# Kernel tuning notes

Measured on AMD Instinct MI355X. Metric: run time of the kernel, lower is better.

The kernel has to match this reference:

```python
import jax, jax.numpy as jnp
import numpy as np

N = 50000       # num_nodes
E = 800000      # num_edges (avg degree 16)
IN, HID, OUT = 128, 128, 128
ALPHA = 0.5
EPS = 1e-5      # torch BatchNorm1d default eps


def _lin_init(k, fan_in, fan_out):
    # mimic torch nn.Linear default init: U(-1/sqrt(fan_in), 1/sqrt(fan_in))
    s = 1.0 / np.sqrt(fan_in)
    kw, kb = jax.random.split(k)
    W = jax.random.uniform(kw, (fan_out, fan_in), jnp.float32, -s, s)
    b = jax.random.uniform(kb, (fan_out,), jnp.float32, -s, s)
    return W, b


def setup_inputs() -> dict:
    key = jax.random.key(0)
    ks = jax.random.split(key, 6)
    x = jax.random.normal(ks[0], (N, IN), jnp.float32)
    edge_index = jax.random.randint(ks[1], (2, E), 0, N, dtype=jnp.int64)
    W1, b1 = _lin_init(ks[2], IN, HID)
    W2, b2 = _lin_init(ks[3], HID, HID)
    W3, b3 = _lin_init(ks[4], HID, OUT)
    g1 = jnp.ones((HID,), jnp.float32); bt1 = jnp.zeros((HID,), jnp.float32)
    g2 = jnp.ones((HID,), jnp.float32); bt2 = jnp.zeros((HID,), jnp.float32)
    return {"x": x, "edge_index": edge_index,
            "W1": W1, "b1": b1, "W2": W2, "b2": b2, "W3": W3, "b3": b3,
            "g1": g1, "bt1": bt1, "g2": g2, "bt2": bt2}


def _high_pass(h, row, col):
    # (I - alpha * A_norm) h, with GCN-style symmetric normalization
    # deg computed from row (source) indices, as in the torch code.
    deg = jax.ops.segment_sum(jnp.ones((E,), h.dtype), row, num_segments=N)
    dinv = jnp.where(deg > 0, deg ** -0.5, 0.0)   # [N]
    norm = dinv[row] * dinv[col]                  # [E]
    agg = jax.ops.segment_sum(h[col] * norm[:, None], row, num_segments=N)
    return h - ALPHA * agg


def _bn(h, g, b):
    # BatchNorm1d in training mode: batch statistics (biased variance)
    m = h.mean(axis=0)
    v = h.var(axis=0)
    return (h - m) * jax.lax.rsqrt(v + EPS) * g + b


def reference(x, edge_index, W1, b1, W2, b2, W3, b3, g1, bt1, g2, bt2):
    row, col = edge_index[0], edge_index[1]
    # layer 0
    h = _high_pass(x, row, col)
    h = h @ W1.T + b1
    h = jax.nn.relu(_bn(h, g1, bt1))  # dropout is identity at eval
    # layer 1
    h = _high_pass(h, row, col)
    h = h @ W2.T + b2
    h = jax.nn.relu(_bn(h, g2, bt2))
    # layer 2 (output)
    h = _high_pass(h, row, col)
    h = h @ W3.T + b3
    return h
```

## Files before the change

### kernel.cpp

```cpp
#include <hip/hip_runtime.h>
#include <hip/hip_fp16.h>

#define N_NODES 50000
#define N_EDGES 800000
#define F 128
#define ALPHA 0.5f
#define BN_EPS 1e-5f
#define NB_SCAN ((N_NODES + 255) / 256)
#define GEMM_NBLK ((N_NODES + 63) / 64)
#define NGRP 8
#define GRP_ROWS (N_NODES / NGRP)
#define NCHUNK 64
#define CHUNK_I4 (N_EDGES / NCHUNK / 4)
#define PREP_THREADS 1024
#define NB_X2H ((N_NODES * F / 8 + PREP_THREADS - 1) / PREP_THREADS)
#define NB_PB 6
#define NB_HIST (NGRP * NCHUNK)

typedef _Float16 half8_t __attribute__((ext_vector_type(8)));
typedef float floatx4 __attribute__((ext_vector_type(4)));

union H8 { uint4 u; __half2 h2[4]; };

__global__ __launch_bounds__(PREP_THREADS) void prep_kernel(
        const float* __restrict__ x, __half* __restrict__ xh,
        const float* __restrict__ W1, const float* __restrict__ W2,
        const float* __restrict__ W3, _Float16* __restrict__ Bp,
        const int* __restrict__ row, int* __restrict__ subhist) {
    int bid = blockIdx.x;
    if (bid < NB_X2H) {
        int idx = bid * PREP_THREADS + threadIdx.x;
        if (idx < N_NODES * F / 8) {
            float4 f0 = ((const float4*)x)[idx * 2];
            float4 f1 = ((const float4*)x)[idx * 2 + 1];
            H8 o;
            o.h2[0] = __float22half2_rn(make_float2(f0.x, f0.y));
            o.h2[1] = __float22half2_rn(make_float2(f0.z, f0.w));
            o.h2[2] = __float22half2_rn(make_float2(f1.x, f1.y));
            o.h2[3] = __float22half2_rn(make_float2(f1.z, f1.w));
            ((uint4*)xh)[idx] = o.u;
        }
    } else if (bid < NB_X2H + NB_PB) {
        int idx = (bid - NB_X2H) * PREP_THREADS + threadIdx.x;
        int layer = idx >> 11;
        int r = idx & 2047;
        int t = r >> 6, lane = r & 63;
        int s = t >> 3, n0 = t & 7;
        int n = n0 * 16 + (lane & 15);
        int k = s * 32 + (lane >> 4) * 8;
        const float* W = (layer == 0) ? W1 : (layer == 1) ? W2 : W3;
        float4 f0 = *(const float4*)(W + n * 128 + k);
        float4 f1 = *(const float4*)(W + n * 128 + k + 4);
        _Float16* dst = Bp + (size_t)layer * 32768 + (size_t)r * 8;
        dst[0] = (_Float16)f0.x; dst[1] = (_Float16)f0.y;
        dst[2] = (_Float16)f0.z; dst[3] = (_Float16)f0.w;
        dst[4] = (_Float16)f1.x; dst[5] = (_Float16)f1.y;
        dst[6] = (_Float16)f1.z; dst[7] = (_Float16)f1.w;
    } else {
        int t = bid - (NB_X2H + NB_PB);
        int g = t & 7, c = t >> 3;
        int rlo = g * GRP_ROWS;
        __shared__ int hist[GRP_ROWS];
        for (int j = threadIdx.x; j < GRP_ROWS; j += PREP_THREADS) hist[j] = 0;
        __syncthreads();
        const int4* r4 = (const int4*)row;
        for (int v = c * CHUNK_I4 + threadIdx.x; v < (c + 1) * CHUNK_I4;
             v += PREP_THREADS) {
            int4 rr = r4[v];
            if ((unsigned)(rr.x - rlo) < GRP_ROWS) atomicAdd(&hist[rr.x - rlo], 1);
            if ((unsigned)(rr.y - rlo) < GRP_ROWS) atomicAdd(&hist[rr.y - rlo], 1);
            if ((unsigned)(rr.z - rlo) < GRP_ROWS) atomicAdd(&hist[rr.z - rlo], 1);
            if ((unsigned)(rr.w - rlo) < GRP_ROWS) atomicAdd(&hist[rr.w - rlo], 1);
        }
        __syncthreads();
        for (int j = threadIdx.x; j < GRP_ROWS; j += PREP_THREADS)
            subhist[(size_t)c * N_NODES + rlo + j] = hist[j];
    }
}


__global__ void scan_block(int* __restrict__ subhist, int* __restrict__ localscan,
                           int* __restrict__ blocksum, float* __restrict__ dinv) {
    __shared__ int s[256];
    int i = blockIdx.x * 256 + threadIdx.x;
    int deg = 0;
    if (i < N_NODES) {
        for (int c = 0; c < NCHUNK; ++c) {
            int t = subhist[(size_t)c * N_NODES + i];
            subhist[(size_t)c * N_NODES + i] = deg;
            deg += t;
        }
        dinv[i] = deg > 0 ? rsqrtf((float)deg) : 0.f;
    }
    s[threadIdx.x] = deg;
    __syncthreads();
    for (int off = 1; off < 256; off <<= 1) {
        int t = (threadIdx.x >= off) ? s[threadIdx.x - off] : 0;
        __syncthreads();
        s[threadIdx.x] += t;
        __syncthreads();
    }
    if (i < N_NODES) localscan[i] = s[threadIdx.x];
    if (threadIdx.x == 255) blocksum[blockIdx.x] = s[255];
}

__global__ void scan_add_tops(const int* __restrict__ localscan,
                              const int* __restrict__ blocksum,
                              int* __restrict__ rowptr) {
    __shared__ int s[256];
    int v = (threadIdx.x < NB_SCAN) ? blocksum[threadIdx.x] : 0;
    s[threadIdx.x] = v;
    __syncthreads();
    for (int off = 1; off < 256; off <<= 1) {
        int t = (threadIdx.x >= off) ? s[threadIdx.x - off] : 0;
        __syncthreads();
        s[threadIdx.x] += t;
        __syncthreads();
    }
    int base = (blockIdx.x > 0) ? s[blockIdx.x - 1] : 0;
    int i = blockIdx.x * 256 + threadIdx.x;
    if (i < N_NODES) rowptr[i + 1] = localscan[i] + base;
    if (i == 0) rowptr[0] = 0;
}


__global__ __launch_bounds__(PREP_THREADS) void fill_kernel(
        const int* __restrict__ row, const int* __restrict__ col,
        const int* __restrict__ rowptr, const int* __restrict__ chunkoff,
        const float* __restrict__ dinv, unsigned int* __restrict__ colwt) {
    int t = blockIdx.x;
    int g = t & 7, c = t >> 3;
    int rlo = g * GRP_ROWS;
    __shared__ int cur[GRP_ROWS];
    for (int j = threadIdx.x; j < GRP_ROWS; j += PREP_THREADS)
        cur[j] = rowptr[rlo + j] + chunkoff[(size_t)c * N_NODES + rlo + j];
    __syncthreads();
    const int4* r4 = (const int4*)row;
    const int4* c4 = (const int4*)col;
    for (int v = c * CHUNK_I4 + threadIdx.x; v < (c + 1) * CHUNK_I4;
         v += PREP_THREADS) {
        int4 rr = r4[v];
        int4 cc = c4[v];
        int rs[4] = {rr.x, rr.y, rr.z, rr.w};
        int cs[4] = {cc.x, cc.y, cc.z, cc.w};
        #pragma unroll
        for (int k = 0; k < 4; ++k) {
            if ((unsigned)(rs[k] - rlo) < GRP_ROWS) {
                int pos = atomicAdd(&cur[rs[k] - rlo], 1);
                unsigned int hb = __half_as_ushort(__float2half(dinv[cs[k]]));
                colwt[pos] = (unsigned int)cs[k] | (hb << 16);
            }
        }
    }
}

template <int USEBN>
__global__ __launch_bounds__(256) void hp_kernel(
        const __half* __restrict__ h,
        const float* __restrict__ scale, const float* __restrict__ shift,
        const float* __restrict__ dinv, const int* __restrict__ rowptr,
        const unsigned int* __restrict__ colwt, __half* __restrict__ out) {
    int lane = threadIdx.x & 63;
    int q = lane >> 4;
    int l = lane & 15;
    int i = blockIdx.x * 4 + (threadIdx.x >> 6);

    float sc[8], sh[8];
    if (USEBN) {
        float4 a0 = ((const float4*)scale)[l * 2];
        float4 a1 = ((const float4*)scale)[l * 2 + 1];
        float4 b0 = ((const float4*)shift)[l * 2];
        float4 b1 = ((const float4*)shift)[l * 2 + 1];
        sc[0] = a0.x; sc[1] = a0.y; sc[2] = a0.z; sc[3] = a0.w;
        sc[4] = a1.x; sc[5] = a1.y; sc[6] = a1.z; sc[7] = a1.w;
        sh[0] = b0.x; sh[1] = b0.y; sh[2] = b0.z; sh[3] = b0.w;
        sh[4] = b1.x; sh[5] = b1.y; sh[6] = b1.z; sh[7] = b1.w;
    }

    int e0 = rowptr[i], e1 = rowptr[i + 1];
    const char* hb = (const char*)h;
    int loff = l * 16;
    float acc[8] = {0.f, 0.f, 0.f, 0.f, 0.f, 0.f, 0.f, 0.f};

    int e = e0 + q;
    for (; e + 4 < e1; e += 8) {
        unsigned int cw0 = colwt[e];
        unsigned int cw1 = colwt[e + 4];
        H8 r0, r1;
        r0.u = *(const uint4*)(hb + (size_t)(cw0 & 0xffffu) * 256 + loff);
        r1.u = *(const uint4*)(hb + (size_t)(cw1 & 0xffffu) * 256 + loff);
        float w0 = __half2float(__ushort_as_half((unsigned short)(cw0 >> 16)));
        float w1 = __half2float(__ushort_as_half((unsigned short)(cw1 >> 16)));
        #pragma unroll
        for (int p = 0; p < 4; ++p) {
            float2 f0 = __half22float2(r0.h2[p]);
            float2 f1 = __half22float2(r1.h2[p]);
            if (USEBN) {
                f0.x = fmaxf(fmaf(f0.x, sc[2 * p], sh[2 * p]), 0.f);
                f0.y = fmaxf(fmaf(f0.y, sc[2 * p + 1], sh[2 * p + 1]), 0.f);
                f1.x = fmaxf(fmaf(f1.x, sc[2 * p], sh[2 * p]), 0.f);
                f1.y = fmaxf(fmaf(f1.y, sc[2 * p + 1], sh[2 * p + 1]), 0.f);
            }
            acc[2 * p]     = fmaf(w0, f0.x, acc[2 * p]);
            acc[2 * p + 1] = fmaf(w0, f0.y, acc[2 * p + 1]);
            acc[2 * p]     = fmaf(w1, f1.x, acc[2 * p]);
            acc[2 * p + 1] = fmaf(w1, f1.y, acc[2 * p + 1]);
        }
    }
    for (; e < e1; e += 4) {
        unsigned int cw = colwt[e];
        H8 r0;
        r0.u = *(const uint4*)(hb + (size_t)(cw & 0xffffu) * 256 + loff);
        float w0 = __half2float(__ushort_as_half((unsigned short)(cw >> 16)));
        #pragma unroll
        for (int p = 0; p < 4; ++p) {
            float2 f0 = __half22float2(r0.h2[p]);
            if (USEBN) {
                f0.x = fmaxf(fmaf(f0.x, sc[2 * p], sh[2 * p]), 0.f);
                f0.y = fmaxf(fmaf(f0.y, sc[2 * p + 1], sh[2 * p + 1]), 0.f);
            }
            acc[2 * p]     = fmaf(w0, f0.x, acc[2 * p]);
            acc[2 * p + 1] = fmaf(w0, f0.y, acc[2 * p + 1]);
        }
    }

    #pragma unroll
    for (int c = 0; c < 8; ++c) {
        acc[c] += __shfl_xor(acc[c], 16);
        acc[c] += __shfl_xor(acc[c], 32);
    }

    float a = ALPHA * dinv[i];
    if (q == 0) {
        H8 s8, o;
        s8.u = *(const uint4*)(hb + (size_t)i * 256 + loff);
        #pragma unroll
        for (int p = 0; p < 4; ++p) {
            float2 f = __half22float2(s8.h2[p]);
            if (USEBN) {
                f.x = fmaxf(fmaf(f.x, sc[2 * p], sh[2 * p]), 0.f);
                f.y = fmaxf(fmaf(f.y, sc[2 * p + 1], sh[2 * p + 1]), 0.f);
            }
            o.h2[p] = __float22half2_rn(
                make_float2(f.x - a * acc[2 * p], f.y - a * acc[2 * p + 1]));
        }
        *(uint4*)((char*)out + (size_t)i * 256 + loff) = o.u;
    }
}

template <int MODE>
__global__ __launch_bounds__(256) void gemm_kernel(
        const __half* __restrict__ A, const _Float16* __restrict__ Bp,
        const float* __restrict__ bias, void* __restrict__ outv,
        float* __restrict__ partial, int M) {
    __shared__ float st_s[4][128];
    __shared__ float st_q[4][128];
    int tid = threadIdx.x;
    int w = tid >> 6, lane = tid & 63;
    int l = lane & 15, g = lane >> 4;
    int row0 = blockIdx.x * 64 + w * 16;
    bool active = row0 < M;

    const char* Ab = (const char*)A;
    half8_t a[4];
    if (active) {
        #pragma unroll
        for (int s = 0; s < 4; ++s)
            a[s] = *(const half8_t*)(Ab + (size_t)(row0 + l) * 256 + s * 64 + g * 16);
    } else {
        half8_t z = 0;
        a[0] = z; a[1] = z; a[2] = z; a[3] = z;
    }

    #pragma unroll
    for (int n0 = 0; n0 < 8; ++n0) {
        floatx4 acc = {0.f, 0.f, 0.f, 0.f};
        #pragma unroll
        for (int s = 0; s < 4; ++s) {
            half8_t b = *(const half8_t*)(Bp + ((size_t)(s * 8 + n0) * 64 + lane) * 8);
            acc = __builtin_amdgcn_mfma_f32_16x16x32_f16(a[s], b, acc, 0, 0, 0);
        }
        int col = n0 * 16 + l;
        float bv = bias[col];
        float v0 = acc[0] + bv, v1 = acc[1] + bv, v2 = acc[2] + bv, v3 = acc[3] + bv;
        if (active) {
            int r = row0 + g * 4;
            if (MODE == 0) {
                __half* oh = (__half*)outv;
                oh[(size_t)r * 128 + col]       = __float2half_rn(v0);
                oh[(size_t)(r + 1) * 128 + col] = __float2half_rn(v1);
                oh[(size_t)(r + 2) * 128 + col] = __float2half_rn(v2);
                oh[(size_t)(r + 3) * 128 + col] = __float2half_rn(v3);
            } else {
                float* of = (float*)outv;
                of[(size_t)r * 128 + col]       = v0;
                of[(size_t)(r + 1) * 128 + col] = v1;
                of[(size_t)(r + 2) * 128 + col] = v2;
                of[(size_t)(r + 3) * 128 + col] = v3;
            }
        } else {
            v0 = v1 = v2 = v3 = 0.f;
        }
        if (MODE == 0) {
            float s_ = v0 + v1 + v2 + v3;
            float q_ = v0 * v0 + v1 * v1 + v2 * v2 + v3 * v3;
            s_ += __shfl_xor(s_, 16); s_ += __shfl_xor(s_, 32);
            q_ += __shfl_xor(q_, 16); q_ += __shfl_xor(q_, 32);
            if (lane < 16) { st_s[w][col] = s_; st_q[w][col] = q_; }
        }
    }
    if (MODE == 0) {
        __syncthreads();
        if (tid < 128) {
            partial[(size_t)blockIdx.x * 256 + tid] =
                st_s[0][tid] + st_s[1][tid] + st_s[2][tid] + st_s[3][tid];
            partial[(size_t)blockIdx.x * 256 + 128 + tid] =
                st_q[0][tid] + st_q[1][tid] + st_q[2][tid] + st_q[3][tid];
        }
    }
}

__global__ __launch_bounds__(256) void bn_reduce_kernel(
        const float* __restrict__ partial,
        const float* __restrict__ g, const float* __restrict__ bt,
        float* __restrict__ scale, float* __restrict__ shift) {
    __shared__ float ss[256], sq[256];
    int j = blockIdx.x;
    int tid = threadIdx.x;
    float s = 0.f, q = 0.f;
    for (int b = tid; b < GEMM_NBLK; b += 256) {
        s += partial[(size_t)b * 256 + j];
        q += partial[(size_t)b * 256 + 128 + j];
    }
    ss[tid] = s; sq[tid] = q;
    __syncthreads();
    for (int off = 128; off > 0; off >>= 1) {
        if (tid < off) { ss[tid] += ss[tid + off]; sq[tid] += sq[tid + off]; }
        __syncthreads();
    }
    if (tid == 0) {
        float m = ss[0] / (float)N_NODES;
        float v = sq[0] / (float)N_NODES - m * m;
        float sc = g[j] * rsqrtf(v + BN_EPS);
        scale[j] = sc;
        shift[j] = bt[j] - m * sc;
    }
}


extern "C" void kernel_launch(void* const* d_in, const int* in_sizes, int n_in,
                              void* d_out, int out_size, void* d_ws, size_t ws_size,
                              hipStream_t stream) {
    const float* x   = (const float*)d_in[0];
    const int*   ei  = (const int*)d_in[1];
    const float* W1  = (const float*)d_in[2];
    const float* b1  = (const float*)d_in[3];
    const float* W2  = (const float*)d_in[4];
    const float* b2  = (const float*)d_in[5];
    const float* W3  = (const float*)d_in[6];
    const float* b3  = (const float*)d_in[7];
    const float* g1  = (const float*)d_in[8];
    const float* bt1 = (const float*)d_in[9];
    const float* g2  = (const float*)d_in[10];
    const float* bt2 = (const float*)d_in[11];
    float* out = (float*)d_out;

    const int* row = ei;
    const int* col = ei + N_EDGES;

    char* ws = (char*)d_ws;
    size_t off = 0;
    auto alloc = [&](size_t bytes) -> void* {
        void* p = ws + off;
        off += (bytes + 255) & ~(size_t)255;
        return p;
    };
    int*   rowptr   = (int*)alloc((N_NODES + 1) * 4);
    int*   localscan= (int*)alloc(N_NODES * 4);
    int*   blocksum = (int*)alloc(NB_SCAN * 4);
    float* dinv     = (float*)alloc(N_NODES * 4);
    unsigned int* colwt = (unsigned int*)alloc((size_t)N_EDGES * 4);
    _Float16* Bp    = (_Float16*)alloc(3 * 32768 * 2);
    float* partial  = (float*)alloc((size_t)GEMM_NBLK * 256 * 4);
    float* scale1   = (float*)alloc(F * 4);
    float* shift1   = (float*)alloc(F * 4);
    float* scale2   = (float*)alloc(F * 4);
    float* shift2   = (float*)alloc(F * 4);
    __half* xh      = (__half*)alloc((size_t)N_NODES * F * 2);
    __half* hpA     = (__half*)alloc((size_t)(N_NODES + 64) * F * 2);
    __half* hB      = (__half*)alloc((size_t)N_NODES * F * 2);
    int* subhist    = (int*)hB;
    (void)ws_size; (void)n_in; (void)in_sizes; (void)out_size;

    prep_kernel<<<NB_X2H + NB_PB + NB_HIST, PREP_THREADS, 0, stream>>>(
        x, xh, W1, W2, W3, Bp, row, subhist);
    scan_block<<<NB_SCAN, 256, 0, stream>>>(subhist, localscan, blocksum, dinv);
    scan_add_tops<<<NB_SCAN, 256, 0, stream>>>(localscan, blocksum, rowptr);
    fill_kernel<<<NB_HIST, PREP_THREADS, 0, stream>>>(row, col, rowptr, subhist,
                                                      dinv, colwt);

    const int hp_grid = N_NODES / 4;

    hp_kernel<0><<<hp_grid, 256, 0, stream>>>(xh, nullptr, nullptr, dinv, rowptr,
                                              colwt, hpA);
    gemm_kernel<0><<<GEMM_NBLK, 256, 0, stream>>>(hpA, Bp, b1, hB, partial, N_NODES);
    bn_reduce_kernel<<<128, 256, 0, stream>>>(partial, g1, bt1, scale1, shift1);

    hp_kernel<1><<<hp_grid, 256, 0, stream>>>(hB, scale1, shift1, dinv, rowptr,
                                              colwt, hpA);
    gemm_kernel<0><<<GEMM_NBLK, 256, 0, stream>>>(hpA, Bp + 32768, b2, hB, partial,
                                                  N_NODES);
    bn_reduce_kernel<<<128, 256, 0, stream>>>(partial, g2, bt2, scale2, shift2);

    hp_kernel<1><<<hp_grid, 256, 0, stream>>>(hB, scale2, shift2, dinv, rowptr,
                                              colwt, hpA);
    gemm_kernel<1><<<GEMM_NBLK, 256, 0, stream>>>(hpA, Bp + 65536, b3, out, nullptr,
                                                  N_NODES);
}
```

Before: 190.8 us.

## Fuse high-pass aggregation with MFMA GEMM through an LDS tile

Merges each layer's sparse high-pass gather and the following dense GEMM into one kernel. Each block aggregates 64 rows, with each wave handling 16 rows in turn, and writes them into a swizzled shared-memory tile that feeds the MFMA GEMM directly. This removes the fp16 intermediate buffer round trip through global memory and one launch per layer. The gather loop is also unrolled to four edges per lane. The cost is far fewer waves in flight (one block per 64 rows instead of per 4 rows), which may reduce latency hiding for the irregular gathers.

```diff
diff --git a/kernel.cpp b/kernel.cpp
--- a/kernel.cpp
+++ b/kernel.cpp
@@ -154,137 +154,164 @@
     }
 }
 
-template <int USEBN>
-__global__ __launch_bounds__(256) void hp_kernel(
+template <int USEBN, int MODE>
+__global__ __launch_bounds__(256) void fused_kernel(
         const __half* __restrict__ h,
         const float* __restrict__ scale, const float* __restrict__ shift,
         const float* __restrict__ dinv, const int* __restrict__ rowptr,
-        const unsigned int* __restrict__ colwt, __half* __restrict__ out) {
-    int lane = threadIdx.x & 63;
-    int q = lane >> 4;
-    int l = lane & 15;
-    int i = blockIdx.x * 4 + (threadIdx.x >> 6);
-
-    float sc[8], sh[8];
-    if (USEBN) {
-        float4 a0 = ((const float4*)scale)[l * 2];
-        float4 a1 = ((const float4*)scale)[l * 2 + 1];
-        float4 b0 = ((const float4*)shift)[l * 2];
-        float4 b1 = ((const float4*)shift)[l * 2 + 1];
-        sc[0] = a0.x; sc[1] = a0.y; sc[2] = a0.z; sc[3] = a0.w;
-        sc[4] = a1.x; sc[5] = a1.y; sc[6] = a1.z; sc[7] = a1.w;
-        sh[0] = b0.x; sh[1] = b0.y; sh[2] = b0.z; sh[3] = b0.w;
-        sh[4] = b1.x; sh[5] = b1.y; sh[6] = b1.z; sh[7] = b1.w;
-    }
-
-    int e0 = rowptr[i], e1 = rowptr[i + 1];
-    const char* hb = (const char*)h;
-    int loff = l * 16;
-    float acc[8] = {0.f, 0.f, 0.f, 0.f, 0.f, 0.f, 0.f, 0.f};
-
-    int e = e0 + q;
-    for (; e + 4 < e1; e += 8) {
-        unsigned int cw0 = colwt[e];
-        unsigned int cw1 = colwt[e + 4];
-        H8 r0, r1;
-        r0.u = *(const uint4*)(hb + (size_t)(cw0 & 0xffffu) * 256 + loff);
-        r1.u = *(const uint4*)(hb + (size_t)(cw1 & 0xffffu) * 256 + loff);
-        float w0 = __half2float(__ushort_as_half((unsigned short)(cw0 >> 16)));
-        float w1 = __half2float(__ushort_as_half((unsigned short)(cw1 >> 16)));
-        #pragma unroll
-        for (int p = 0; p < 4; ++p) {
-            float2 f0 = __half22float2(r0.h2[p]);
-            float2 f1 = __half22float2(r1.h2[p]);
-            if (USEBN) {
-                f0.x = fmaxf(fmaf(f0.x, sc[2 * p], sh[2 * p]), 0.f);
-                f0.y = fmaxf(fmaf(f0.y, sc[2 * p + 1], sh[2 * p + 1]), 0.f);
-                f1.x = fmaxf(fmaf(f1.x, sc[2 * p], sh[2 * p]), 0.f);
-                f1.y = fmaxf(fmaf(f1.y, sc[2 * p + 1], sh[2 * p + 1]), 0.f);
-            }
-            acc[2 * p]     = fmaf(w0, f0.x, acc[2 * p]);
-            acc[2 * p + 1] = fmaf(w0, f0.y, acc[2 * p + 1]);
-            acc[2 * p]     = fmaf(w1, f1.x, acc[2 * p]);
-            acc[2 * p + 1] = fmaf(w1, f1.y, acc[2 * p + 1]);
-        }
-    }
-    for (; e < e1; e += 4) {
-        unsigned int cw = colwt[e];
-        H8 r0;
-        r0.u = *(const uint4*)(hb + (size_t)(cw & 0xffffu) * 256 + loff);
-        float w0 = __half2float(__ushort_as_half((unsigned short)(cw >> 16)));
-        #pragma unroll
-        for (int p = 0; p < 4; ++p) {
-            float2 f0 = __half22float2(r0.h2[p]);
-            if (USEBN) {
-                f0.x = fmaxf(fmaf(f0.x, sc[2 * p], sh[2 * p]), 0.f);
-                f0.y = fmaxf(fmaf(f0.y, sc[2 * p + 1], sh[2 * p + 1]), 0.f);
-            }
-            acc[2 * p]     = fmaf(w0, f0.x, acc[2 * p]);
-            acc[2 * p + 1] = fmaf(w0, f0.y, acc[2 * p + 1]);
-        }
-    }
-
-    #pragma unroll
-    for (int c = 0; c < 8; ++c) {
-        acc[c] += __shfl_xor(acc[c], 16);
-        acc[c] += __shfl_xor(acc[c], 32);
-    }
-
-    float a = ALPHA * dinv[i];
-    if (q == 0) {
-        H8 s8, o;
-        s8.u = *(const uint4*)(hb + (size_t)i * 256 + loff);
-        #pragma unroll
-        for (int p = 0; p < 4; ++p) {
-            float2 f = __half22float2(s8.h2[p]);
-            if (USEBN) {
-                f.x = fmaxf(fmaf(f.x, sc[2 * p], sh[2 * p]), 0.f);
-                f.y = fmaxf(fmaf(f.y, sc[2 * p + 1], sh[2 * p + 1]), 0.f);
-            }
-            o.h2[p] = __float22half2_rn(
-                make_float2(f.x - a * acc[2 * p], f.y - a * acc[2 * p + 1]));
-        }
-        *(uint4*)((char*)out + (size_t)i * 256 + loff) = o.u;
-    }
-}
-
-template <int MODE>
-__global__ __launch_bounds__(256) void gemm_kernel(
-        const __half* __restrict__ A, const _Float16* __restrict__ Bp,
-        const float* __restrict__ bias, void* __restrict__ outv,
-        float* __restrict__ partial, int M) {
+        const unsigned int* __restrict__ colwt,
+        const _Float16* __restrict__ Bp, const float* __restrict__ bias,
+        void* __restrict__ outv, float* __restrict__ partial) {
+    __shared__ uint4 sA[64 * 16];
     __shared__ float st_s[4][128];
     __shared__ float st_q[4][128];
     int tid = threadIdx.x;
     int w = tid >> 6, lane = tid & 63;
-    int l = lane & 15, g = lane >> 4;
+    int q = lane >> 4, l = lane & 15;
     int row0 = blockIdx.x * 64 + w * 16;
-    bool active = row0 < M;
-
-    const char* Ab = (const char*)A;
-    half8_t a[4];
+    bool active = row0 < N_NODES;
+
+    const char* hb = (const char*)h;
+    int loff = l * 16;
+
     if (active) {
-        #pragma unroll
-        for (int s = 0; s < 4; ++s)
-            a[s] = *(const half8_t*)(Ab + (size_t)(row0 + l) * 256 + s * 64 + g * 16);
-    } else {
-        half8_t z = 0;
-        a[0] = z; a[1] = z; a[2] = z; a[3] = z;
-    }
-
-    #pragma unroll
-    for (int n0 = 0; n0 < 8; ++n0) {
-        floatx4 acc = {0.f, 0.f, 0.f, 0.f};
+        float sc[8], sh[8];
+        if (USEBN) {
+            float4 a0 = ((const float4*)scale)[l * 2];
+            float4 a1 = ((const float4*)scale)[l * 2 + 1];
+            float4 b0 = ((const float4*)shift)[l * 2];
+            float4 b1 = ((const float4*)shift)[l * 2 + 1];
+            sc[0] = a0.x; sc[1] = a0.y; sc[2] = a0.z; sc[3] = a0.w;
+            sc[4] = a1.x; sc[5] = a1.y; sc[6] = a1.z; sc[7] = a1.w;
+            sh[0] = b0.x; sh[1] = b0.y; sh[2] = b0.z; sh[3] = b0.w;
+            sh[4] = b1.x; sh[5] = b1.y; sh[6] = b1.z; sh[7] = b1.w;
+        }
+        for (int rr = 0; rr < 16; ++rr) {
+            int i = row0 + rr;
+            int e0 = rowptr[i], e1 = rowptr[i + 1];
+            float acc[8] = {0.f, 0.f, 0.f, 0.f, 0.f, 0.f, 0.f, 0.f};
+            int e = e0 + q;
+            for (; e + 14 < e1; e += 16) {
+                unsigned int cw0 = colwt[e];
+                unsigned int cw1 = colwt[e + 4];
+                unsigned int cw2 = colwt[e + 8];
+                unsigned int cw3 = colwt[e + 12];
+                H8 r0, r1, r2, r3;
+                r0.u = *(const uint4*)(hb + (size_t)(cw0 & 0xffffu) * 256 + loff);
+                r1.u = *(const uint4*)(hb + (size_t)(cw1 & 0xffffu) * 256 + loff);
+                r2.u = *(const uint4*)(hb + (size_t)(cw2 & 0xffffu) * 256 + loff);
+                r3.u = *(const uint4*)(hb + (size_t)(cw3 & 0xffffu) * 256 + loff);
+                float w0 = __half2float(__ushort_as_half((unsigned short)(cw0 >> 16)));
+                float w1 = __half2float(__ushort_as_half((unsigned short)(cw1 >> 16)));
+                float w2 = __half2float(__ushort_as_half((unsigned short)(cw2 >> 16)));
+                float w3 = __half2float(__ushort_as_half((unsigned short)(cw3 >> 16)));
+                #pragma unroll
+                for (int p = 0; p < 4; ++p) {
+                    float2 f0 = __half22float2(r0.h2[p]);
+                    float2 f1 = __half22float2(r1.h2[p]);
+                    float2 f2 = __half22float2(r2.h2[p]);
+                    float2 f3 = __half22float2(r3.h2[p]);
+                    if (USEBN) {
+                        f0.x = fmaxf(fmaf(f0.x, sc[2 * p], sh[2 * p]), 0.f);
+                        f0.y = fmaxf(fmaf(f0.y, sc[2 * p + 1], sh[2 * p + 1]), 0.f);
+                        f1.x = fmaxf(fmaf(f1.x, sc[2 * p], sh[2 * p]), 0.f);
+                        f1.y = fmaxf(fmaf(f1.y, sc[2 * p + 1], sh[2 * p + 1]), 0.f);
+                        f2.x = fmaxf(fmaf(f2.x, sc[2 * p], sh[2 * p]), 0.f);
+                        f2.y = fmaxf(fmaf(f2.y, sc[2 * p + 1], sh[2 * p + 1]), 0.f);
+                        f3.x = fmaxf(fmaf(f3.x, sc[2 * p], sh[2 * p]), 0.f);
+                        f3.y = fmaxf(fmaf(f3.y, sc[2 * p + 1], sh[2 * p + 1]), 0.f);
+                    }
+                    acc[2 * p]     = fmaf(w0, f0.x, acc[2 * p]);
+                    acc[2 * p + 1] = fmaf(w0, f0.y, acc[2 * p + 1]);
+                    acc[2 * p]     = fmaf(w1, f1.x, acc[2 * p]);
+                    acc[2 * p + 1] = fmaf(w1, f1.y, acc[2 * p + 1]);
+                    acc[2 * p]     = fmaf(w2, f2.x, acc[2 * p]);
+                    acc[2 * p + 1] = fmaf(w2, f2.y, acc[2 * p + 1]);
+                    acc[2 * p]     = fmaf(w3, f3.x, acc[2 * p]);
+                    acc[2 * p + 1] = fmaf(w3, f3.y, acc[2 * p + 1]);
+                }
+            }
+            for (; e + 6 < e1; e += 8) {
+                unsigned int cw0 = colwt[e];
+                unsigned int cw1 = colwt[e + 4];
+                H8 r0, r1;
+                r0.u = *(const uint4*)(hb + (size_t)(cw0 & 0xffffu) * 256 + loff);
+                r1.u = *(const uint4*)(hb + (size_t)(cw1 & 0xffffu) * 256 + loff);
+                float w0 = __half2float(__ushort_as_half((unsigned short)(cw0 >> 16)));
+                float w1 = __half2float(__ushort_as_half((unsigned short)(cw1 >> 16)));
+                #pragma unroll
+                for (int p = 0; p < 4; ++p) {
+                    float2 f0 = __half22float2(r0.h2[p]);
+                    float2 f1 = __half22float2(r1.h2[p]);
+                    if (USEBN) {
+                        f0.x = fmaxf(fmaf(f0.x, sc[2 * p], sh[2 * p]), 0.f);
+                        f0.y = fmaxf(fmaf(f0.y, sc[2 * p + 1], sh[2 * p + 1]), 0.f);
+                        f1.x = fmaxf(fmaf(f1.x, sc[2 * p], sh[2 * p]), 0.f);
+                        f1.y = fmaxf(fmaf(f1.y, sc[2 * p + 1], sh[2 * p + 1]), 0.f);
+                    }
+                    acc[2 * p]     = fmaf(w0, f0.x, acc[2 * p]);
+                    acc[2 * p + 1] = fmaf(w0, f0.y, acc[2 * p + 1]);
+                    acc[2 * p]     = fmaf(w1, f1.x, acc[2 * p]);
+                    acc[2 * p + 1] = fmaf(w1, f1.y, acc[2 * p + 1]);
+                }
+            }
+            for (; e < e1; e += 4) {
+                unsigned int cw = colwt[e];
+                H8 r0;
+                r0.u = *(const uint4*)(hb + (size_t)(cw & 0xffffu) * 256 + loff);
+                float w0 = __half2float(__ushort_as_half((unsigned short)(cw >> 16)));
+                #pragma unroll
+                for (int p = 0; p < 4; ++p) {
+                    float2 f0 = __half22float2(r0.h2[p]);
+                    if (USEBN) {
+                        f0.x = fmaxf(fmaf(f0.x, sc[2 * p], sh[2 * p]), 0.f);
+                        f0.y = fmaxf(fmaf(f0.y, sc[2 * p + 1], sh[2 * p + 1]), 0.f);
+                    }
+                    acc[2 * p]     = fmaf(w0, f0.x, acc[2 * p]);
+                    acc[2 * p + 1] = fmaf(w0, f0.y, acc[2 * p + 1]);
+                }
+            }
+            #pragma unroll
+            for (int c = 0; c < 8; ++c) {
+                acc[c] += __shfl_xor(acc[c], 16);
+                acc[c] += __shfl_xor(acc[c], 32);
+            }
+            if (q == 0) {
+                float a = ALPHA * dinv[i];
+                H8 s8, o;
+                s8.u = *(const uint4*)(hb + (size_t)i * 256 + loff);
+                #pragma unroll
+                for (int p = 0; p < 4; ++p) {
+                    float2 f = __half22float2(s8.h2[p]);
+                    if (USEBN) {
+                        f.x = fmaxf(fmaf(f.x, sc[2 * p], sh[2 * p]), 0.f);
+                        f.y = fmaxf(fmaf(f.y, sc[2 * p + 1], sh[2 * p + 1]), 0.f);
+                    }
+                    o.h2[p] = __float22half2_rn(
+                        make_float2(f.x - a * acc[2 * p], f.y - a * acc[2 * p + 1]));
+                }
+                sA[(w * 16 + rr) * 16 + (l ^ (rr & 7))] = o.u;
+            }
+        }
+        int g2 = lane >> 4;
+        half8_t a[4];
         #pragma unroll
         for (int s = 0; s < 4; ++s) {
-            half8_t b = *(const half8_t*)(Bp + ((size_t)(s * 8 + n0) * 64 + lane) * 8);
-            acc = __builtin_amdgcn_mfma_f32_16x16x32_f16(a[s], b, acc, 0, 0, 0);
-        }
-        int col = n0 * 16 + l;
-        float bv = bias[col];
-        float v0 = acc[0] + bv, v1 = acc[1] + bv, v2 = acc[2] + bv, v3 = acc[3] + bv;
-        if (active) {
-            int r = row0 + g * 4;
+            int chunk = (s * 4 + g2) ^ (l & 7);
+            a[s] = *(const half8_t*)&sA[(w * 16 + l) * 16 + chunk];
+        }
+        #pragma unroll
+        for (int n0 = 0; n0 < 8; ++n0) {
+            floatx4 acc = {0.f, 0.f, 0.f, 0.f};
+            #pragma unroll
+            for (int s = 0; s < 4; ++s) {
+                half8_t b = *(const half8_t*)(Bp + ((size_t)(s * 8 + n0) * 64 + lane) * 8);
+                acc = __builtin_amdgcn_mfma_f32_16x16x32_f16(a[s], b, acc, 0, 0, 0);
+            }
+            int col = n0 * 16 + l;
+            float bv = bias[col];
+            float v0 = acc[0] + bv, v1 = acc[1] + bv, v2 = acc[2] + bv, v3 = acc[3] + bv;
+            int r = row0 + g2 * 4;
             if (MODE == 0) {
                 __half* oh = (__half*)outv;
                 oh[(size_t)r * 128 + col]       = __float2half_rn(v0);
@@ -298,15 +325,21 @@
                 of[(size_t)(r + 2) * 128 + col] = v2;
                 of[(size_t)(r + 3) * 128 + col] = v3;
             }
-        } else {
-            v0 = v1 = v2 = v3 = 0.f;
-        }
-        if (MODE == 0) {
-            float s_ = v0 + v1 + v2 + v3;
-            float q_ = v0 * v0 + v1 * v1 + v2 * v2 + v3 * v3;
-            s_ += __shfl_xor(s_, 16); s_ += __shfl_xor(s_, 32);
-            q_ += __shfl_xor(q_, 16); q_ += __shfl_xor(q_, 32);
-            if (lane < 16) { st_s[w][col] = s_; st_q[w][col] = q_; }
+            if (MODE == 0) {
+                float s_ = v0 + v1 + v2 + v3;
+                float q_ = v0 * v0 + v1 * v1 + v2 * v2 + v3 * v3;
+                s_ += __shfl_xor(s_, 16); s_ += __shfl_xor(s_, 32);
+                q_ += __shfl_xor(q_, 16); q_ += __shfl_xor(q_, 32);
+                if (lane < 16) { st_s[w][col] = s_; st_q[w][col] = q_; }
+            }
+        }
+    } else if (MODE == 0) {
+        if (lane < 16) {
+            #pragma unroll
+            for (int n0 = 0; n0 < 8; ++n0) {
+                st_s[w][n0 * 16 + l] = 0.f;
+                st_q[w][n0 * 16 + l] = 0.f;
+            }
         }
     }
     if (MODE == 0) {
@@ -387,9 +420,9 @@
     float* scale2   = (float*)alloc(F * 4);
     float* shift2   = (float*)alloc(F * 4);
     __half* xh      = (__half*)alloc((size_t)N_NODES * F * 2);
-    __half* hpA     = (__half*)alloc((size_t)(N_NODES + 64) * F * 2);
-    __half* hB      = (__half*)alloc((size_t)N_NODES * F * 2);
-    int* subhist    = (int*)hB;
+    __half* h1      = (__half*)alloc((size_t)N_NODES * F * 2);
+    __half* h2      = (__half*)alloc((size_t)N_NODES * F * 2);
+    int* subhist    = (int*)h1;
     (void)ws_size; (void)n_in; (void)in_sizes; (void)out_size;
 
     prep_kernel<<<NB_X2H + NB_PB + NB_HIST, PREP_THREADS, 0, stream>>>(
@@ -399,21 +432,14 @@
     fill_kernel<<<NB_HIST, PREP_THREADS, 0, stream>>>(row, col, rowptr, subhist,
                                                       dinv, colwt);
 
-    const int hp_grid = N_NODES / 4;
-
-    hp_kernel<0><<<hp_grid, 256, 0, stream>>>(xh, nullptr, nullptr, dinv, rowptr,
-                                              colwt, hpA);
-    gemm_kernel<0><<<GEMM_NBLK, 256, 0, stream>>>(hpA, Bp, b1, hB, partial, N_NODES);
+    fused_kernel<0, 0><<<GEMM_NBLK, 256, 0, stream>>>(
+        xh, nullptr, nullptr, dinv, rowptr, colwt, Bp, b1, h1, partial);
     bn_reduce_kernel<<<128, 256, 0, stream>>>(partial, g1, bt1, scale1, shift1);
 
-    hp_kernel<1><<<hp_grid, 256, 0, stream>>>(hB, scale1, shift1, dinv, rowptr,
-                                              colwt, hpA);
-    gemm_kernel<0><<<GEMM_NBLK, 256, 0, stream>>>(hpA, Bp + 32768, b2, hB, partial,
-                                                  N_NODES);
+    fused_kernel<1, 0><<<GEMM_NBLK, 256, 0, stream>>>(
+        h1, scale1, shift1, dinv, rowptr, colwt, Bp + 32768, b2, h2, partial);
     bn_reduce_kernel<<<128, 256, 0, stream>>>(partial, g2, bt2, scale2, shift2);
 
-    hp_kernel<1><<<hp_grid, 256, 0, stream>>>(hB, scale2, shift2, dinv, rowptr,
-                                              colwt, hpA);
-    gemm_kernel<1><<<GEMM_NBLK, 256, 0, stream>>>(hpA, Bp + 65536, b3, out, nullptr,
-                                                  N_NODES);
-}
+    fused_kernel<1, 1><<<GEMM_NBLK, 256, 0, stream>>>(
+        h2, scale2, shift2, dinv, rowptr, colwt, Bp + 65536, b3, out, nullptr);
+}
```

Result: slower. 239.0 us (+25.3%).

## Split node features into 32-column planes so neighbor gathers stay L2-resident

Applied to the files above, without the earlier changes.

Stores the half-precision feature matrices as four column planes of 32 features each. The prep, hp and gemm kernels all index the new layout. The hp grid now runs tile-major, so each aggregation pass gathers from a single 3.2 MB plane that can stay resident in L2, and each wave processes 16 edges at a time with 64-byte rows. The goal is to cut DRAM/L2 misses from the random neighbor gather. In exchange, the CSR index and weight arrays are read four times per layer, and gathers use smaller 64-byte row segments.

```diff
diff --git a/kernel.cpp b/kernel.cpp
--- a/kernel.cpp
+++ b/kernel.cpp
@@ -16,6 +16,10 @@
 #define NB_X2H ((N_NODES * F / 8 + PREP_THREADS - 1) / PREP_THREADS)
 #define NB_PB 6
 #define NB_HIST (NGRP * NCHUNK)
+#define NTILE 4
+#define TILE_C 32
+#define PLANE_H ((size_t)N_NODES * TILE_C)
+#define NRB (N_NODES / 4)
 
 typedef _Float16 half8_t __attribute__((ext_vector_type(8)));
 typedef float floatx4 __attribute__((ext_vector_type(4)));
@@ -31,6 +35,8 @@
     if (bid < NB_X2H) {
         int idx = bid * PREP_THREADS + threadIdx.x;
         if (idx < N_NODES * F / 8) {
+            int i = idx >> 4;
+            int j0 = (idx * 8) & 127;
             float4 f0 = ((const float4*)x)[idx * 2];
             float4 f1 = ((const float4*)x)[idx * 2 + 1];
             H8 o;
@@ -38,7 +44,8 @@
             o.h2[1] = __float22half2_rn(make_float2(f0.z, f0.w));
             o.h2[2] = __float22half2_rn(make_float2(f1.x, f1.y));
             o.h2[3] = __float22half2_rn(make_float2(f1.z, f1.w));
-            ((uint4*)xh)[idx] = o.u;
+            size_t u4 = (size_t)(j0 >> 5) * (PLANE_H / 8) + (size_t)i * 4 + ((j0 & 31) >> 3);
+            ((uint4*)xh)[u4] = o.u;
         }
     } else if (bid < NB_X2H + NB_PB) {
         int idx = (bid - NB_X2H) * PREP_THREADS + threadIdx.x;
@@ -160,17 +167,22 @@
         const float* __restrict__ scale, const float* __restrict__ shift,
         const float* __restrict__ dinv, const int* __restrict__ rowptr,
         const unsigned int* __restrict__ colwt, __half* __restrict__ out) {
+    int t = blockIdx.x / NRB;
+    int rb = blockIdx.x - t * NRB;
     int lane = threadIdx.x & 63;
-    int q = lane >> 4;
-    int l = lane & 15;
-    int i = blockIdx.x * 4 + (threadIdx.x >> 6);
+    int slot = lane >> 2, sub = lane & 3;
+    int i = rb * 4 + (threadIdx.x >> 6);
+
+    const char* plane = (const char*)(h + (size_t)t * PLANE_H);
+    char* oplane = (char*)(out + (size_t)t * PLANE_H);
+    int soff = sub * 16;
 
     float sc[8], sh[8];
     if (USEBN) {
-        float4 a0 = ((const float4*)scale)[l * 2];
-        float4 a1 = ((const float4*)scale)[l * 2 + 1];
-        float4 b0 = ((const float4*)shift)[l * 2];
-        float4 b1 = ((const float4*)shift)[l * 2 + 1];
+        float4 a0 = *(const float4*)(scale + t * TILE_C + sub * 8);
+        float4 a1 = *(const float4*)(scale + t * TILE_C + sub * 8 + 4);
+        float4 b0 = *(const float4*)(shift + t * TILE_C + sub * 8);
+        float4 b1 = *(const float4*)(shift + t * TILE_C + sub * 8 + 4);
         sc[0] = a0.x; sc[1] = a0.y; sc[2] = a0.z; sc[3] = a0.w;
         sc[4] = a1.x; sc[5] = a1.y; sc[6] = a1.z; sc[7] = a1.w;
         sh[0] = b0.x; sh[1] = b0.y; sh[2] = b0.z; sh[3] = b0.w;
@@ -178,17 +190,15 @@
     }
 
     int e0 = rowptr[i], e1 = rowptr[i + 1];
-    const char* hb = (const char*)h;
-    int loff = l * 16;
     float acc[8] = {0.f, 0.f, 0.f, 0.f, 0.f, 0.f, 0.f, 0.f};
 
-    int e = e0 + q;
-    for (; e + 4 < e1; e += 8) {
+    int e = e0 + slot;
+    for (; e + 16 < e1; e += 32) {
         unsigned int cw0 = colwt[e];
-        unsigned int cw1 = colwt[e + 4];
+        unsigned int cw1 = colwt[e + 16];
         H8 r0, r1;
-        r0.u = *(const uint4*)(hb + (size_t)(cw0 & 0xffffu) * 256 + loff);
-        r1.u = *(const uint4*)(hb + (size_t)(cw1 & 0xffffu) * 256 + loff);
+        r0.u = *(const uint4*)(plane + (size_t)(cw0 & 0xffffu) * 64 + soff);
+        r1.u = *(const uint4*)(plane + (size_t)(cw1 & 0xffffu) * 64 + soff);
         float w0 = __half2float(__ushort_as_half((unsigned short)(cw0 >> 16)));
         float w1 = __half2float(__ushort_as_half((unsigned short)(cw1 >> 16)));
         #pragma unroll
@@ -207,10 +217,10 @@
             acc[2 * p + 1] = fmaf(w1, f1.y, acc[2 * p + 1]);
         }
     }
-    for (; e < e1; e += 4) {
+    for (; e < e1; e += 16) {
         unsigned int cw = colwt[e];
         H8 r0;
-        r0.u = *(const uint4*)(hb + (size_t)(cw & 0xffffu) * 256 + loff);
+        r0.u = *(const uint4*)(plane + (size_t)(cw & 0xffffu) * 64 + soff);
         float w0 = __half2float(__ushort_as_half((unsigned short)(cw >> 16)));
         #pragma unroll
         for (int p = 0; p < 4; ++p) {
@@ -226,14 +236,16 @@
 
     #pragma unroll
     for (int c = 0; c < 8; ++c) {
+        acc[c] += __shfl_xor(acc[c], 4);
+        acc[c] += __shfl_xor(acc[c], 8);
         acc[c] += __shfl_xor(acc[c], 16);
         acc[c] += __shfl_xor(acc[c], 32);
     }
 
-    float a = ALPHA * dinv[i];
-    if (q == 0) {
+    if (slot == 0) {
+        float a = ALPHA * dinv[i];
         H8 s8, o;
-        s8.u = *(const uint4*)(hb + (size_t)i * 256 + loff);
+        s8.u = *(const uint4*)(plane + (size_t)i * 64 + soff);
         #pragma unroll
         for (int p = 0; p < 4; ++p) {
             float2 f = __half22float2(s8.h2[p]);
@@ -244,7 +256,7 @@
             o.h2[p] = __float22half2_rn(
                 make_float2(f.x - a * acc[2 * p], f.y - a * acc[2 * p + 1]));
         }
-        *(uint4*)((char*)out + (size_t)i * 256 + loff) = o.u;
+        *(uint4*)(oplane + (size_t)i * 64 + soff) = o.u;
     }
 }
 
@@ -266,7 +278,8 @@
     if (active) {
         #pragma unroll
         for (int s = 0; s < 4; ++s)
-            a[s] = *(const half8_t*)(Ab + (size_t)(row0 + l) * 256 + s * 64 + g * 16);
+            a[s] = *(const half8_t*)(Ab + (size_t)s * PLANE_H * 2 +
+                                     (size_t)(row0 + l) * 64 + g * 16);
     } else {
         half8_t z = 0;
         a[0] = z; a[1] = z; a[2] = z; a[3] = z;
@@ -286,11 +299,12 @@
         if (active) {
             int r = row0 + g * 4;
             if (MODE == 0) {
-                __half* oh = (__half*)outv;
-                oh[(size_t)r * 128 + col]       = __float2half_rn(v0);
-                oh[(size_t)(r + 1) * 128 + col] = __float2half_rn(v1);
-                oh[(size_t)(r + 2) * 128 + col] = __float2half_rn(v2);
-                oh[(size_t)(r + 3) * 128 + col] = __float2half_rn(v3);
+                __half* op = (__half*)outv + (size_t)(col >> 5) * PLANE_H;
+                int cc = col & 31;
+                op[(size_t)r * 32 + cc]       = __float2half_rn(v0);
+                op[(size_t)(r + 1) * 32 + cc] = __float2half_rn(v1);
+                op[(size_t)(r + 2) * 32 + cc] = __float2half_rn(v2);
+                op[(size_t)(r + 3) * 32 + cc] = __float2half_rn(v3);
             } else {
                 float* of = (float*)outv;
                 of[(size_t)r * 128 + col]       = v0;
@@ -387,7 +401,7 @@
     float* scale2   = (float*)alloc(F * 4);
     float* shift2   = (float*)alloc(F * 4);
     __half* xh      = (__half*)alloc((size_t)N_NODES * F * 2);
-    __half* hpA     = (__half*)alloc((size_t)(N_NODES + 64) * F * 2);
+    __half* hpA     = (__half*)alloc((size_t)N_NODES * F * 2);
     __half* hB      = (__half*)alloc((size_t)N_NODES * F * 2);
     int* subhist    = (int*)hB;
     (void)ws_size; (void)n_in; (void)in_sizes; (void)out_size;
@@ -399,7 +413,7 @@
     fill_kernel<<<NB_HIST, PREP_THREADS, 0, stream>>>(row, col, rowptr, subhist,
                                                       dinv, colwt);
 
-    const int hp_grid = N_NODES / 4;
+    const int hp_grid = NTILE * NRB;
 
     hp_kernel<0><<<hp_grid, 256, 0, stream>>>(xh, nullptr, nullptr, dinv, rowptr,
                                               colwt, hpA);
```

Result: slower. 319.2 us (+67.3%).
